# Performance work log

Measured on AMD Instinct MI355X. Metric: run time of the kernel, lower is better.

Reference implementation:

```python
import jax, jax.numpy as jnp
import numpy as np
import math

D = 768
H = 12
DH = D // H
L = 2
EPS = 1e-12
NEG = -10000.0


def layer_norm(x, w, b):
    u = jnp.mean(x, axis=-1, keepdims=True)
    s = jnp.mean((x - u) ** 2, axis=-1, keepdims=True)
    return w * ((x - u) / jnp.sqrt(s + EPS)) + b


def mha(q_in, k_in, v_in, mask, qw, qb, kw, kb, vw, vb):
    # q_in: (B,Lq,D); k_in/v_in: (B,Lk,D); mask: (B,Lq,Lk) or (B,1,Lk)
    B, Lq, _ = q_in.shape
    def proj(x, w, b):
        y = x @ w.T + b
        return y.reshape(x.shape[0], x.shape[1], H, DH).transpose(0, 2, 1, 3)
    q = proj(q_in, qw, qb)  # (B,H,Lq,DH)
    k = proj(k_in, kw, kb)
    v = proj(v_in, vw, vb)
    scores = jnp.einsum('bhqd,bhkd->bhqk', q, k) / math.sqrt(DH)
    scores = scores + (1.0 - mask[:, None]) * NEG  # additive mask, (B,1,Lq,Lk) broadcast
    probs = jax.nn.softmax(scores, axis=-1)
    ctx = jnp.einsum('bhqk,bhkd->bhqd', probs, v)
    return ctx.transpose(0, 2, 1, 3).reshape(B, Lq, D)


def setup_inputs() -> dict:
    key = jax.random.key(0)
    ks = jax.random.split(key, 8)
    B, Lt, Lv = 8, 1024, 512
    inp = {
        'dec_hidden_states': jax.random.normal(ks[0], (B, Lt, D), jnp.float32),
        'dec_mask': jnp.ones((B, Lt), jnp.float32),
        'enc_outputs': jax.random.normal(ks[1], (B, Lv, D), jnp.float32),
        'enc_mask': jnp.ones((B, Lv), jnp.float32),
    }
    wkeys = jax.random.split(ks[2], 7)
    names = ['sa_qw', 'sa_kw', 'sa_vw', 'ca_qw', 'ca_kw', 'ca_vw', 'out_w']
    for n, k in zip(names, wkeys):
        inp[n] = 0.02 * jax.random.normal(k, (L, D, D), jnp.float32)
    for n in ['sa_qb', 'sa_kb', 'sa_vb', 'ca_qb', 'ca_kb', 'ca_vb', 'out_b', 'n1_b', 'n2_b', 'n3_b']:
        inp[n] = jnp.zeros((L, D), jnp.float32)
    for n in ['n1_w', 'n2_w', 'n3_w']:
        inp[n] = jnp.ones((L, D), jnp.float32)
    return inp


def reference(dec_hidden_states, dec_mask, enc_outputs, enc_mask,
              sa_qw, sa_qb, sa_kw, sa_kb, sa_vw, sa_vb, n1_w, n1_b,
              ca_qw, ca_qb, ca_kw, ca_kb, ca_vw, ca_vb, n2_w, n2_b,
              out_w, out_b, n3_w, n3_b):
    Lt = dec_hidden_states.shape[1]
    causal = jnp.tril(jnp.ones((Lt, Lt), dec_mask.dtype))
    self_mask = dec_mask[:, None, :] * causal[None]        # (B,Lt,Lt)
    cross_mask = enc_mask[:, None, :]                      # (B,1,Lv)

    params = (sa_qw, sa_qb, sa_kw, sa_kb, sa_vw, sa_vb, n1_w, n1_b,
              ca_qw, ca_qb, ca_kw, ca_kb, ca_vw, ca_vb, n2_w, n2_b,
              out_w, out_b, n3_w, n3_b)

    def body(x, p):
        (qw, qb, kw, kb, vw, vb, w1, b1,
         cqw, cqb, ckw, ckb, cvw, cvb, w2, b2,
         ow, ob, w3, b3) = p
        a = mha(x, x, x, self_mask, qw, qb, kw, kb, vw, vb)
        x1 = layer_norm(a + x, w1, b1)
        c = mha(x1, enc_outputs, enc_outputs, cross_mask, cqw, cqb, ckw, ckb, cvw, cvb)
        x2 = layer_norm(x1 + c, w2, b2)
        # BertOutput called with (x2, x2): LN(dense(x2) + x2)
        y = layer_norm(x2 @ ow.T + ob + x2, w3, b3)
        return y, None

    out, _ = jax.lax.scan(body, dec_hidden_states, params)
    return out
```

## Files before the change

### kernel.cpp

```cpp
#include <hip/hip_runtime.h>
#include <hip/hip_bf16.h>

#define DMODEL 768
#define NH 12
#define DH 64
#define NEGC -10000.0f

#define AS1 __attribute__((address_space(1)))
#define AS3 __attribute__((address_space(3)))

typedef __bf16 bf16_t;
typedef __bf16 bf16x8 __attribute__((ext_vector_type(8)));
typedef float f32x4 __attribute__((ext_vector_type(4)));

__device__ __forceinline__ f32x4 mfma16(bf16x8 a, bf16x8 b, f32x4 c) {
    return __builtin_amdgcn_mfma_f32_16x16x32_bf16(a, b, c, 0, 0, 0);
}

__device__ __forceinline__ void gl_lds16(const bf16_t* g, void* l) {
    __builtin_amdgcn_global_load_lds((const AS1 void*)g, (AS3 void*)l, 16, 0, 0);
}

__global__ void probe_kernel(const unsigned int* m, int* flag) {
    *flag = (m[0] == 0x3F803F80u) ? 1 : 0;
}

__device__ __forceinline__ void cvt_group(const void* src, bf16_t* dst, int g, int isbf16) {
    if (isbf16) {
        ((bf16x8*)dst)[g] = ((const bf16x8*)src)[g];
    } else {
        const float* s = (const float*)src + (size_t)g * 8;
        bf16x8 v;
#pragma unroll
        for (int i = 0; i < 8; i++) v[i] = (bf16_t)s[i];
        ((bf16x8*)dst)[g] = v;
    }
}

__global__ __launch_bounds__(256) void cvt_kernel(const void* src, bf16_t* dst,
                                                  const int* flag, int n) {
    int g = blockIdx.x * 256 + threadIdx.x;
    if (g * 8 >= n) return;
    cvt_group(src, dst, g, *flag);
}

__global__ __launch_bounds__(256) void cvt7_kernel(
    const void* s0, const void* s1, const void* s2, const void* s3,
    const void* s4, const void* s5, const void* s6,
    bf16_t* dst, const int* flag)
{
    const void* srcs[7] = {s0, s1, s2, s3, s4, s5, s6};
    const void* src = srcs[blockIdx.y];
    bf16_t* d = dst + (size_t)blockIdx.y * 1179648;
    int g = blockIdx.x * 256 + threadIdx.x;
    cvt_group(src, d, g, *flag);
}

__global__ __launch_bounds__(256) void cvt13_kernel(
    const void* s0, const void* s1, const void* s2, const void* s3,
    const void* s4, const void* s5, const void* s6, const void* s7,
    const void* s8, const void* s9, const void* s10, const void* s11,
    const void* s12, bf16_t* dst, const int* flag)
{
    const void* srcs[13] = {s0, s1, s2, s3, s4, s5, s6, s7, s8, s9, s10, s11, s12};
    const void* src = srcs[blockIdx.x];
    bf16_t* d = dst + (size_t)blockIdx.x * 1536;
    int g = threadIdx.x;
    if (g >= 192) return;
    cvt_group(src, d, g, *flag);
}

__global__ __launch_bounds__(256) void gemm128_kernel(
    const bf16_t* __restrict__ X,
    const bf16_t* __restrict__ W0, const bf16_t* __restrict__ W1,
    const bf16_t* __restrict__ W2,
    const bf16_t* __restrict__ B0, const bf16_t* __restrict__ B1,
    const bf16_t* __restrict__ B2,
    bf16_t* __restrict__ O0, bf16_t* __restrict__ O1, bf16_t* __restrict__ O2,
    int M, int vz, int lkShift)
{
    __shared__ __attribute__((aligned(16))) bf16_t alds[128 * 64];
    __shared__ __attribute__((aligned(16))) bf16_t blds[128 * 64];

    const int tid  = threadIdx.x;
    const int lane = tid & 63;
    const int w    = tid >> 6;
    const int r    = lane & 15;
    const int q4   = lane >> 4;
    const int z    = blockIdx.z;
    const int row0 = blockIdx.y * 128;
    const int col0 = blockIdx.x * 128;
    const int wrow = (w >> 1) * 64;
    const int wcol = (w & 1) * 64;

    const bf16_t* W    = (z == 0) ? W0 : ((z == 1) ? W1 : W2);
    const bf16_t* bias = (z == 0) ? B0 : ((z == 1) ? B1 : B2);
    bf16_t*       out  = (z == 0) ? O0 : ((z == 1) ? O1 : O2);
    const int     mode = (z == vz) ? 1 : 0;

    const f32x4 zero4 = {0.f, 0.f, 0.f, 0.f};
    f32x4 acc[4][4];
#pragma unroll
    for (int i = 0; i < 4; i++)
#pragma unroll
        for (int j = 0; j < 4; j++) acc[i][j] = zero4;

    const int srow = (w * 256 + lane) >> 3;
    const int sgc  = (lane & 7) ^ (srow & 7);
    const bf16_t* Xs = X + (size_t)(row0 + srow) * DMODEL + sgc * 8;
    const bf16_t* Ws = W + (size_t)(col0 + srow) * DMODEL + sgc * 8;

    for (int kb = 0; kb < DMODEL; kb += 64) {
        __syncthreads();
#pragma unroll
        for (int j = 0; j < 4; j++) {
            char* la = (char*)alds + w * 4096 + j * 1024;
            char* lb = (char*)blds + w * 4096 + j * 1024;
            gl_lds16(Xs + (size_t)(j * 8) * DMODEL + kb, la);
            gl_lds16(Ws + (size_t)(j * 8) * DMODEL + kb, lb);
        }
        __syncthreads();

#pragma unroll
        for (int ks = 0; ks < 2; ks++) {
            bf16x8 af[4], bf[4];
#pragma unroll
            for (int i = 0; i < 4; i++) {
                int rr_ = wrow + i * 16 + r;
                int pc  = (ks * 4 + q4) ^ (rr_ & 7);
                af[i] = *(const bf16x8*)&alds[rr_ * 64 + pc * 8];
            }
#pragma unroll
            for (int j = 0; j < 4; j++) {
                int cc_ = wcol + j * 16 + r;
                int pc  = (ks * 4 + q4) ^ (cc_ & 7);
                bf[j] = *(const bf16x8*)&blds[cc_ * 64 + pc * 8];
            }
#pragma unroll
            for (int i = 0; i < 4; i++)
#pragma unroll
                for (int j = 0; j < 4; j++)
                    acc[i][j] = mfma16(af[i], bf[j], acc[i][j]);
        }
    }

#pragma unroll
    for (int i = 0; i < 4; i++)
#pragma unroll
        for (int j = 0; j < 4; j++)
#pragma unroll
            for (int rr = 0; rr < 4; rr++) {
                int grow = row0 + wrow + i * 16 + q4 * 4 + rr;
                int gcol = col0 + wcol + j * 16 + r;
                float v = acc[i][j][rr] + (float)bias[gcol];
                if (mode == 0) {
                    out[(size_t)grow * DMODEL + gcol] = (bf16_t)v;
                } else {
                    int bidx = grow >> lkShift;
                    int t    = grow & ((1 << lkShift) - 1);
                    int h    = gcol >> 6;
                    int dd   = gcol & 63;
                    out[((size_t)((bidx * NH + h) * 64 + dd) << lkShift) + t] = (bf16_t)v;
                }
            }
}

__global__ __launch_bounds__(256) void attn_kernel(
    const bf16_t* Q, const bf16_t* __restrict__ K,
    const bf16_t* __restrict__ Vt, const bf16_t* __restrict__ mask,
    bf16_t* ctx, int Lq, int Lk, int causal)
{
    __shared__ __attribute__((aligned(16))) bf16_t kvlds[2][2][4096];
    __shared__ __attribute__((aligned(16))) bf16_t plds[4][1024];
    const int tid  = threadIdx.x;
    const int lane = tid & 63;
    const int wv   = tid >> 6;
    const int r    = lane & 15;
    const int q4   = lane >> 4;
    const int b    = blockIdx.z;
    const int h    = blockIdx.y;
    const int qblk = (gridDim.x - 1 - blockIdx.x) * 64;
    const int qbase = qblk + wv * 16;

    const bf16_t* Qp = Q + ((size_t)(b * Lq + qbase + r)) * DMODEL + h * DH + q4 * 8;
    bf16x8 qf0 = *(const bf16x8*)(Qp);
    bf16x8 qf1 = *(const bf16x8*)(Qp + 32);
    const bf16_t* Kg = K + ((size_t)b * Lk) * DMODEL + h * DH;
    const bf16_t* Vg = Vt + ((size_t)(b * NH + h) * DH) * Lk;
    const bf16_t* mp = mask + (size_t)b * Lk;

    const f32x4 zero4 = {0.f, 0.f, 0.f, 0.f};
    float psum[4] = {0.f, 0.f, 0.f, 0.f};
    f32x4 o[4] = {zero4, zero4, zero4, zero4};

    const int nt = causal ? ((qblk >> 6) + 1) : (Lk >> 6);

    auto stage = [&](int buf, int kb) {
#pragma unroll
        for (int j = 0; j < 2; j++) {
            gl_lds16(Kg + (size_t)(kb + wv * 16 + r) * DMODEL + (j * 4 + q4) * 8,
                     &kvlds[buf][0][wv * 1024 + j * 512]);
            gl_lds16(Vg + (size_t)(wv * 16 + r) * Lk + kb + (j * 4 + q4) * 8,
                     &kvlds[buf][1][wv * 1024 + j * 512]);
        }
    };

    stage(0, 0);
    for (int i = 0; i < nt; i++) {
        const int kb  = i << 6;
        const int cur = i & 1;
        asm volatile("s_waitcnt lgkmcnt(0)" ::: "memory");
        __builtin_amdgcn_s_barrier();
        float mb[4];
#pragma unroll
        for (int t = 0; t < 4; t++)
            mb[t] = (1.f - (float)mp[kb + t * 16 + r]) * NEGC;
        if (i + 1 < nt) {
            stage(cur ^ 1, kb + 64);
            asm volatile("s_waitcnt vmcnt(4)" ::: "memory");
        } else {
            asm volatile("s_waitcnt vmcnt(0)" ::: "memory");
        }
        __builtin_amdgcn_s_barrier();

        const bf16_t* kl = kvlds[cur][0];
        const bf16_t* vl = kvlds[cur][1];
        f32x4 s[4];
#pragma unroll
        for (int t = 0; t < 4; t++) {
            bf16x8 k0 = *(const bf16x8*)&kl[t * 1024 + lane * 8];
            bf16x8 k1 = *(const bf16x8*)&kl[t * 1024 + 512 + lane * 8];
            s[t] = mfma16(qf1, k1, mfma16(qf0, k0, zero4));
        }
#pragma unroll
        for (int t = 0; t < 4; t++) {
#pragma unroll
            for (int rr = 0; rr < 4; rr++) {
                float f = s[t][rr] * 0.125f + mb[t];
                float pv = __expf(f);
                if (causal && kb + t * 16 + r > qbase + q4 * 4 + rr) pv = 0.f;
                psum[rr] += pv;
                plds[wv][(t * 2 + (r >> 3)) * 128 + (q4 * 4 + rr) * 8 + (r & 7)] =
                    (bf16_t)pv;
            }
        }
        bf16x8 pa0 = *(const bf16x8*)&plds[wv][lane * 8];
        bf16x8 pa1 = *(const bf16x8*)&plds[wv][512 + lane * 8];
#pragma unroll
        for (int nc = 0; nc < 4; nc++) {
            bf16x8 v0 = *(const bf16x8*)&vl[nc * 1024 + lane * 8];
            bf16x8 v1 = *(const bf16x8*)&vl[nc * 1024 + 512 + lane * 8];
            o[nc] = mfma16(pa1, v1, mfma16(pa0, v0, o[nc]));
        }
    }

#pragma unroll
    for (int rr = 0; rr < 4; rr++) {
        psum[rr] += __shfl_xor(psum[rr], 1, 64);
        psum[rr] += __shfl_xor(psum[rr], 2, 64);
        psum[rr] += __shfl_xor(psum[rr], 4, 64);
        psum[rr] += __shfl_xor(psum[rr], 8, 64);
    }
#pragma unroll
    for (int nc = 0; nc < 4; nc++)
#pragma unroll
        for (int rr = 0; rr < 4; rr++) {
            int qi = qbase + q4 * 4 + rr;
            ctx[((size_t)(b * Lq + qi)) * DMODEL + h * DH + nc * 16 + r] =
                (bf16_t)(o[nc][rr] / psum[rr]);
        }
}

__global__ __launch_bounds__(256) void ln_kernel(
    const bf16_t* a, const bf16_t* res,
    const bf16_t* __restrict__ w, const bf16_t* __restrict__ b,
    void* out, int fin, const int* __restrict__ flag)
{
    __shared__ float red[8];
    const int row = blockIdx.x;
    const int tid = threadIdx.x;
    const int lane = tid & 63;
    const int wv = tid >> 6;
    const bf16_t* ap = a + (size_t)row * DMODEL;
    const bf16_t* rp = res + (size_t)row * DMODEL;
    const int outf32 = fin && (*flag == 0);

    float v[3];
#pragma unroll
    for (int i = 0; i < 3; i++) {
        int c = tid + i * 256;
        v[i] = (float)ap[c] + (float)rp[c];
    }
    float s = v[0] + v[1] + v[2];
#pragma unroll
    for (int m = 1; m < 64; m <<= 1) s += __shfl_xor(s, m, 64);
    if (lane == 0) red[wv] = s;
    __syncthreads();
    float u = (red[0] + red[1] + red[2] + red[3]) * (1.0f / DMODEL);
    float d0 = v[0] - u, d1 = v[1] - u, d2 = v[2] - u;
    float s2 = d0 * d0 + d1 * d1 + d2 * d2;
#pragma unroll
    for (int m = 1; m < 64; m <<= 1) s2 += __shfl_xor(s2, m, 64);
    if (lane == 0) red[4 + wv] = s2;
    __syncthreads();
    float var = (red[4] + red[5] + red[6] + red[7]) * (1.0f / DMODEL);
    float rstd = rsqrtf(var + 1e-12f);
#pragma unroll
    for (int i = 0; i < 3; i++) {
        int c = tid + i * 256;
        float y = ((v[i] - u) * rstd) * (float)w[c] + (float)b[c];
        if (outf32) ((float*)out)[(size_t)row * DMODEL + c] = y;
        else        ((bf16_t*)out)[(size_t)row * DMODEL + c] = (bf16_t)y;
    }
}

extern "C" void kernel_launch(void* const* d_in, const int* in_sizes, int n_in,
                              void* d_out, int out_size, void* d_ws, size_t ws_size,
                              hipStream_t stream)
{
    const int B = 8, Lt = 1024, Lv = 512;
    const size_t A = (size_t)B * Lt * DMODEL;
    const size_t E = (size_t)B * Lv * DMODEL;
    const size_t WT = 2 * (size_t)DMODEL * DMODEL;
    const int WSZ = DMODEL * DMODEL;

    char* p = (char*)d_ws;
    int* flagp = (int*)p;            p += 64;
    bf16_t* cdec = (bf16_t*)p;       p += A * 2;
    bf16_t* cenc = (bf16_t*)p;       p += E * 2;
    bf16_t* cdm  = (bf16_t*)p;       p += (size_t)B * Lt * 2;
    bf16_t* cem  = (bf16_t*)p;       p += (size_t)B * Lv * 2;
    bf16_t* cw   = (bf16_t*)p;       p += 7 * WT * 2;
    bf16_t* cb   = (bf16_t*)p;       p += 13 * 1536 * 2;
    bf16_t* b0   = (bf16_t*)p;       p += A * 2;
    bf16_t* b1   = (bf16_t*)p;       p += A * 2;
    bf16_t* b2   = (bf16_t*)p;       p += A * 2;
    bf16_t* dob  = (bf16_t*)d_out;

    const bf16_t* sa_qw = cw + 0 * WT, * sa_kw = cw + 1 * WT, * sa_vw = cw + 2 * WT;
    const bf16_t* ca_qw = cw + 3 * WT, * ca_kw = cw + 4 * WT, * ca_vw = cw + 5 * WT;
    const bf16_t* out_w = cw + 6 * WT;
    const bf16_t* sa_qb = cb + 0 * 1536, * sa_kb = cb + 1 * 1536, * sa_vb = cb + 2 * 1536;
    const bf16_t* ca_qb = cb + 3 * 1536, * ca_kb = cb + 4 * 1536, * ca_vb = cb + 5 * 1536;
    const bf16_t* out_b = cb + 6 * 1536;
    const bf16_t* n1_b  = cb + 7 * 1536, * n2_b = cb + 8 * 1536, * n3_b = cb + 9 * 1536;
    const bf16_t* n1_w  = cb + 10 * 1536, * n2_w = cb + 11 * 1536, * n3_w = cb + 12 * 1536;

    probe_kernel<<<1, 1, 0, stream>>>((const unsigned int*)d_in[1], flagp);
    cvt_kernel<<<dim3((unsigned)(A / 2048)), 256, 0, stream>>>(d_in[0], cdec, flagp, (int)A);
    cvt_kernel<<<dim3((unsigned)(E / 2048)), 256, 0, stream>>>(d_in[2], cenc, flagp, (int)E);
    cvt_kernel<<<dim3(4),  256, 0, stream>>>(d_in[1], cdm, flagp, B * Lt);
    cvt_kernel<<<dim3(2),  256, 0, stream>>>(d_in[3], cem, flagp, B * Lv);
    cvt7_kernel<<<dim3(576, 7), 256, 0, stream>>>(
        d_in[4], d_in[5], d_in[6], d_in[7], d_in[8], d_in[9], d_in[10], cw, flagp);
    cvt13_kernel<<<dim3(13), 256, 0, stream>>>(
        d_in[11], d_in[12], d_in[13], d_in[14], d_in[15], d_in[16], d_in[17],
        d_in[18], d_in[19], d_in[20], d_in[21], d_in[22], d_in[23], cb, flagp);

    const int Mdec = B * Lt;
    const int Menc = B * Lv;
    dim3 blk(256);
    dim3 gQKV(DMODEL / 128, Mdec / 128, 3);
    dim3 gOne(DMODEL / 128, Mdec / 128, 1);
    dim3 gKVe(DMODEL / 128, Menc / 128, 2);
    dim3 gAttn(Lt / 64, NH, B);
    dim3 gLN(Mdec);

    for (int l = 0; l < 2; l++) {
        const bf16_t* xin = (l == 0) ? cdec : dob;
        gemm128_kernel<<<gQKV, blk, 0, stream>>>(
            xin, sa_qw + l * WSZ, sa_kw + l * WSZ, sa_vw + l * WSZ,
            sa_qb + l * DMODEL, sa_kb + l * DMODEL, sa_vb + l * DMODEL,
            b0, b1, b2, Mdec, 2, 10);
        attn_kernel<<<gAttn, blk, 0, stream>>>(b0, b1, b2, cdm, b0, Lt, Lt, 1);
        ln_kernel<<<gLN, blk, 0, stream>>>(b0, xin, n1_w + l * DMODEL, n1_b + l * DMODEL, b0, 0, flagp);
        gemm128_kernel<<<gOne, blk, 0, stream>>>(
            b0, ca_qw + l * WSZ, ca_qw, ca_qw,
            ca_qb + l * DMODEL, ca_qb, ca_qb,
            b1, b1, b1, Mdec, -1, 0);
        gemm128_kernel<<<gKVe, blk, 0, stream>>>(
            cenc, ca_kw + l * WSZ, ca_vw + l * WSZ, ca_vw,
            ca_kb + l * DMODEL, ca_vb + l * DMODEL, ca_vb,
            b2, dob, dob, Menc, 1, 9);
        attn_kernel<<<gAttn, blk, 0, stream>>>(b1, b2, dob, cem, b1, Lt, Lv, 0);
        ln_kernel<<<gLN, blk, 0, stream>>>(b1, b0, n2_w + l * DMODEL, n2_b + l * DMODEL, b1, 0, flagp);
        gemm128_kernel<<<gOne, blk, 0, stream>>>(
            b1, out_w + l * WSZ, out_w, out_w,
            out_b + l * DMODEL, out_b, out_b,
            b2, b2, b2, Mdec, -1, 0);
        ln_kernel<<<gLN, blk, 0, stream>>>(b2, b1, n3_w + l * DMODEL, n3_b + l * DMODEL, dob, (l == 1) ? 1 : 0, flagp);
    }
}
```

Baseline: 707.6 us.

## Double-buffer GEMM LDS tiles and remap blocks to XCD-grouped row bands

The GEMM kernel now uses two LDS buffers so the next k-tile's global-to-LDS loads are issued before computing on the current tile, with explicit waitcnt and barriers in place of the old two-syncthreads pattern. The grid becomes 1D and block ids are remapped so each XCD (id & 7) handles a contiguous row band across all column tiles and z-planes. Together these aim to hide global load latency and to improve L2 reuse of the activation rows within an XCD. LDS use doubles, which may lower occupancy, and the remap assumes ny is a multiple of 8.

```diff
diff --git a/kernel.cpp b/kernel.cpp
--- a/kernel.cpp
+++ b/kernel.cpp
@@ -77,21 +77,29 @@
     const bf16_t* __restrict__ B0, const bf16_t* __restrict__ B1,
     const bf16_t* __restrict__ B2,
     bf16_t* __restrict__ O0, bf16_t* __restrict__ O1, bf16_t* __restrict__ O2,
-    int M, int vz, int lkShift)
-{
-    __shared__ __attribute__((aligned(16))) bf16_t alds[128 * 64];
-    __shared__ __attribute__((aligned(16))) bf16_t blds[128 * 64];
+    int nx, int ny, int nz, int vz, int lkShift)
+{
+    __shared__ __attribute__((aligned(16))) bf16_t alds[2][128 * 64];
+    __shared__ __attribute__((aligned(16))) bf16_t blds[2][128 * 64];
 
     const int tid  = threadIdx.x;
     const int lane = tid & 63;
     const int w    = tid >> 6;
     const int r    = lane & 15;
     const int q4   = lane >> 4;
-    const int z    = blockIdx.z;
-    const int row0 = blockIdx.y * 128;
-    const int col0 = blockIdx.x * 128;
-    const int wrow = (w >> 1) * 64;
-    const int wcol = (w & 1) * 64;
+
+    const int id     = blockIdx.x;
+    const int xcd    = id & 7;
+    const int slot   = id >> 3;
+    const int planes = nx * nz;
+    const int band   = xcd + 8 * (slot / planes);
+    const int p      = slot % planes;
+    const int z      = p / nx;
+    const int bx     = p - z * nx;
+    const int row0   = band * 128;
+    const int col0   = bx * 128;
+    const int wrow   = (w >> 1) * 64;
+    const int wcol   = (w & 1) * 64;
 
     const bf16_t* W    = (z == 0) ? W0 : ((z == 1) ? W1 : W2);
     const bf16_t* bias = (z == 0) ? B0 : ((z == 1) ? B1 : B2);
@@ -110,37 +118,52 @@
     const bf16_t* Xs = X + (size_t)(row0 + srow) * DMODEL + sgc * 8;
     const bf16_t* Ws = W + (size_t)(col0 + srow) * DMODEL + sgc * 8;
 
-    for (int kb = 0; kb < DMODEL; kb += 64) {
-        __syncthreads();
+    auto stage = [&](int buf, int kb) {
 #pragma unroll
         for (int j = 0; j < 4; j++) {
-            char* la = (char*)alds + w * 4096 + j * 1024;
-            char* lb = (char*)blds + w * 4096 + j * 1024;
-            gl_lds16(Xs + (size_t)(j * 8) * DMODEL + kb, la);
-            gl_lds16(Ws + (size_t)(j * 8) * DMODEL + kb, lb);
-        }
-        __syncthreads();
-
+            gl_lds16(Xs + (size_t)(j * 8) * DMODEL + kb,
+                     (char*)&alds[buf][0] + w * 4096 + j * 1024);
+            gl_lds16(Ws + (size_t)(j * 8) * DMODEL + kb,
+                     (char*)&blds[buf][0] + w * 4096 + j * 1024);
+        }
+    };
+
+    const int NIT = DMODEL / 64;
+    stage(0, 0);
+    for (int i = 0; i < NIT; i++) {
+        const int cur = i & 1;
+        asm volatile("s_waitcnt lgkmcnt(0)" ::: "memory");
+        __builtin_amdgcn_s_barrier();
+        if (i + 1 < NIT) {
+            stage(cur ^ 1, (i + 1) * 64);
+            asm volatile("s_waitcnt vmcnt(8)" ::: "memory");
+        } else {
+            asm volatile("s_waitcnt vmcnt(0)" ::: "memory");
+        }
+        __builtin_amdgcn_s_barrier();
+
+        const bf16_t* al = alds[cur];
+        const bf16_t* bl = blds[cur];
 #pragma unroll
         for (int ks = 0; ks < 2; ks++) {
             bf16x8 af[4], bf[4];
 #pragma unroll
-            for (int i = 0; i < 4; i++) {
-                int rr_ = wrow + i * 16 + r;
+            for (int ii = 0; ii < 4; ii++) {
+                int rr_ = wrow + ii * 16 + r;
                 int pc  = (ks * 4 + q4) ^ (rr_ & 7);
-                af[i] = *(const bf16x8*)&alds[rr_ * 64 + pc * 8];
+                af[ii] = *(const bf16x8*)&al[rr_ * 64 + pc * 8];
             }
 #pragma unroll
             for (int j = 0; j < 4; j++) {
                 int cc_ = wcol + j * 16 + r;
                 int pc  = (ks * 4 + q4) ^ (cc_ & 7);
-                bf[j] = *(const bf16x8*)&blds[cc_ * 64 + pc * 8];
+                bf[j] = *(const bf16x8*)&bl[cc_ * 64 + pc * 8];
             }
 #pragma unroll
-            for (int i = 0; i < 4; i++)
+            for (int ii = 0; ii < 4; ii++)
 #pragma unroll
                 for (int j = 0; j < 4; j++)
-                    acc[i][j] = mfma16(af[i], bf[j], acc[i][j]);
+                    acc[ii][j] = mfma16(af[ii], bf[j], acc[ii][j]);
         }
     }
 
@@ -360,9 +383,9 @@
     const int Mdec = B * Lt;
     const int Menc = B * Lv;
     dim3 blk(256);
-    dim3 gQKV(DMODEL / 128, Mdec / 128, 3);
-    dim3 gOne(DMODEL / 128, Mdec / 128, 1);
-    dim3 gKVe(DMODEL / 128, Menc / 128, 2);
+    dim3 gQKV(6 * 64 * 3);
+    dim3 gOne(6 * 64 * 1);
+    dim3 gKVe(6 * 32 * 2);
     dim3 gAttn(Lt / 64, NH, B);
     dim3 gLN(Mdec);
 
@@ -371,23 +394,23 @@
         gemm128_kernel<<<gQKV, blk, 0, stream>>>(
             xin, sa_qw + l * WSZ, sa_kw + l * WSZ, sa_vw + l * WSZ,
             sa_qb + l * DMODEL, sa_kb + l * DMODEL, sa_vb + l * DMODEL,
-            b0, b1, b2, Mdec, 2, 10);
+            b0, b1, b2, 6, 64, 3, 2, 10);
         attn_kernel<<<gAttn, blk, 0, stream>>>(b0, b1, b2, cdm, b0, Lt, Lt, 1);
         ln_kernel<<<gLN, blk, 0, stream>>>(b0, xin, n1_w + l * DMODEL, n1_b + l * DMODEL, b0, 0, flagp);
         gemm128_kernel<<<gOne, blk, 0, stream>>>(
             b0, ca_qw + l * WSZ, ca_qw, ca_qw,
             ca_qb + l * DMODEL, ca_qb, ca_qb,
-            b1, b1, b1, Mdec, -1, 0);
+            b1, b1, b1, 6, 64, 1, -1, 0);
         gemm128_kernel<<<gKVe, blk, 0, stream>>>(
             cenc, ca_kw + l * WSZ, ca_vw + l * WSZ, ca_vw,
             ca_kb + l * DMODEL, ca_vb + l * DMODEL, ca_vb,
-            b2, dob, dob, Menc, 1, 9);
+            b2, dob, dob, 6, 32, 2, 1, 9);
         attn_kernel<<<gAttn, blk, 0, stream>>>(b1, b2, dob, cem, b1, Lt, Lv, 0);
         ln_kernel<<<gLN, blk, 0, stream>>>(b1, b0, n2_w + l * DMODEL, n2_b + l * DMODEL, b1, 0, flagp);
         gemm128_kernel<<<gOne, blk, 0, stream>>>(
             b1, out_w + l * WSZ, out_w, out_w,
             out_b + l * DMODEL, out_b, out_b,
-            b2, b2, b2, Mdec, -1, 0);
+            b2, b2, b2, 6, 64, 1, -1, 0);
         ln_kernel<<<gLN, blk, 0, stream>>>(b2, b1, n3_w + l * DMODEL, n3_b + l * DMODEL, dob, (l == 1) ? 1 : 0, flagp);
     }
 }
```

Measured after the change: 701.0 us. No clear change (-0.9%).
